# Optimization experiments

Measured on AMD Instinct MI355X. Metric: run time of the kernel, lower is better.

## Reference

```python
import jax, jax.numpy as jnp
import numpy as np

EPS = 1e-7  # K.epsilon()
ROUTINGS = 3


def squash(v, axis=-1):
    s2 = jnp.sum(jnp.square(v), axis=axis, keepdims=True)
    scale = s2 / (1.0 + s2) / jnp.sqrt(s2 + EPS)
    return scale * v


def setup_inputs() -> dict:
    key = jax.random.key(0)
    k1, k2 = jax.random.split(key)
    B, I, D_IN = 64, 2048, 16
    J, D_OUT = 32, 32
    inputs = jax.random.normal(k1, (B, I, D_IN), dtype=jnp.float32)
    W = jax.random.normal(k2, (J, I, D_OUT, D_IN), dtype=jnp.float32) * 0.05
    return {"inputs": inputs, "W": W}


def reference(inputs, W):
    # u_hat[b,j,i,e] = sum_d inputs[b,i,d] * W[j,i,e,d]
    u_hat = jnp.einsum('bid,jied->bjie', inputs, W)  # [B, J, I, D_out]
    B, J, I, _ = u_hat.shape
    b = jnp.zeros((B, J, I), dtype=u_hat.dtype)
    outputs = None
    for r in range(ROUTINGS):
        c = jax.nn.softmax(b, axis=1)                 # softmax over output capsules J
        s = jnp.einsum('bji,bjie->bje', c, u_hat)     # weighted sum over input capsules
        outputs = squash(s)                           # [B, J, D_out]
        if r < ROUTINGS - 1:
            b = b + jnp.einsum('bje,bjie->bji', outputs, u_hat)
    return outputs
```

## Files before the change

kernel.cpp:

```cpp
#include <hip/hip_runtime.h>
#include <hip/hip_bf16.h>

#define NB 64
#define NI 2048
#define ND 16
#define NJ 32
#define NE 32
#define NIP (NI/2)
#define NKC 64
#define NSL NKC

typedef __attribute__((ext_vector_type(8))) short bfrag;
typedef __attribute__((ext_vector_type(4))) float f32x4;

__device__ inline unsigned pk2bf(float a, float b) {
    __hip_bfloat162 h = __float22bfloat162_rn(make_float2(a, b));
    return *reinterpret_cast<unsigned*>(&h);
}

template <int N>
__device__ inline float rot16_add(float v) {
    int r = __builtin_amdgcn_mov_dpp(__float_as_int(v), 0x120 + N, 0xf, 0xf, false);
    return v + __int_as_float(r);
}

__device__ inline unsigned scale_pair(unsigned u, float cc) {
    float f0 = __uint_as_float(u << 16);
    float f1 = __uint_as_float(u & 0xffff0000u);
    return pk2bf(f0 * cc, f1 * cc);
}

__global__ __launch_bounds__(256) void convxT_k(const float* __restrict__ x,
                                                short* __restrict__ xT)
{
    const int T = blockIdx.x * 256 + threadIdx.x;
    const int i = T >> 6, b = T & 63;
    const float4* src = reinterpret_cast<const float4*>(
        x + ((size_t)b * NI + i) * ND);
    float4 a0 = src[0], a1 = src[1], a2 = src[2], a3 = src[3];
    bfrag lo, hi;
    unsigned* lu = reinterpret_cast<unsigned*>(&lo);
    unsigned* hu = reinterpret_cast<unsigned*>(&hi);
    lu[0] = pk2bf(a0.x, a0.y); lu[1] = pk2bf(a0.z, a0.w);
    lu[2] = pk2bf(a1.x, a1.y); lu[3] = pk2bf(a1.z, a1.w);
    hu[0] = pk2bf(a2.x, a2.y); hu[1] = pk2bf(a2.z, a2.w);
    hu[2] = pk2bf(a3.x, a3.y); hu[3] = pk2bf(a3.z, a3.w);
    short* dst = xT + ((size_t)i * NB + b) * ND;
    *reinterpret_cast<bfrag*>(dst)     = lo;
    *reinterpret_cast<bfrag*>(dst + 8) = hi;
}

__global__ __launch_bounds__(512) void lgsm_k(
    const short* __restrict__ xT,
    const short* __restrict__ Wb,
    const float* __restrict__ Oacc,
    float* __restrict__ c)
{
    const int l    = blockIdx.x;
    const int grp  = l >> 5;
    const int bb   = (l >> 3) & 3;
    const int ic   = grp * 8 + (l & 7);
    const int b0   = bb * 16;
    const int i0   = ic * 16;
    const int t    = threadIdx.x;
    const int wv   = t >> 6;
    const int ln   = t & 63;
    const int m    = ln & 15;
    const int quad = ln >> 4;

    __shared__ float lp[NJ][16][16];

    float O0[4][4], O1[4][4];
#pragma unroll
    for (int jj = 0; jj < 4; ++jj) {
        const int j = wv * 4 + jj;
#pragma unroll
        for (int r = 0; r < 4; ++r) {
            const int b = b0 + quad * 4 + r;
            O0[jj][r] = Oacc[((size_t)b * NJ + j) * NE + m];
            O1[jj][r] = Oacc[((size_t)b * NJ + j) * NE + 16 + m];
        }
    }

    const int  bA  = b0 + m;
    const bool act = quad < 2;
    const int  d0  = quad * 8;

    for (int il = 0; il < 16; ++il) {
        const int i = i0 + il;
        const int ip = i >> 1, isel = i & 1;
        bfrag av = (bfrag)0;
        if (act) {
            av = *reinterpret_cast<const bfrag*>(
                xT + ((size_t)i * NB + bA) * ND + d0);
        }
#pragma unroll
        for (int jj = 0; jj < 4; ++jj) {
            const int j = wv * 4 + jj;
            bfrag bv0 = (bfrag)0, bv1 = (bfrag)0;
            if (act) {
                const short* wp = Wb + (((size_t)j * NIP + ip) * NE + m) * 32
                                     + isel * 16 + d0;
                bv0 = *reinterpret_cast<const bfrag*>(wp);
                bv1 = *reinterpret_cast<const bfrag*>(wp + 16 * 32);
            }
            f32x4 z = {0.f, 0.f, 0.f, 0.f};
            f32x4 U0 = __builtin_amdgcn_mfma_f32_16x16x32_bf16(av, bv0, z, 0, 0, 0);
            f32x4 U1 = __builtin_amdgcn_mfma_f32_16x16x32_bf16(av, bv1, z, 0, 0, 0);

            float v4[4];
#pragma unroll
            for (int r = 0; r < 4; ++r) {
                float v = fmaf(U0[r], O0[jj][r], U1[r] * O1[jj][r]);
                v = rot16_add<1>(v);
                v = rot16_add<2>(v);
                v = rot16_add<4>(v);
                v = rot16_add<8>(v);
                v4[r] = v;
            }
            if (m == 0) {
                *reinterpret_cast<float4*>(&lp[j][il][quad * 4]) =
                    make_float4(v4[0], v4[1], v4[2], v4[3]);
            }
        }
    }
    __syncthreads();

    if (t < 256) {
        const int i = t >> 4, b = t & 15;
        float v[NJ];
        float mx = -1e30f;
#pragma unroll
        for (int jx = 0; jx < NJ; ++jx) {
            v[jx] = lp[jx][i][b];
            mx = fmaxf(mx, v[jx]);
        }
        float sum = 0.f;
#pragma unroll
        for (int jx = 0; jx < NJ; ++jx) {
            v[jx] = __expf(v[jx] - mx);
            sum += v[jx];
        }
        const float inv = 1.0f / sum;
#pragma unroll
        for (int jx = 0; jx < NJ; ++jx)
            c[((size_t)jx * NI + i0 + i) * NB + b0 + b] = v[jx] * inv;
    }
}


#define WS_LOAD(P, itv)                                                        \
    {   const int ip_ = ip0 + (itv);                                           \
        const int ia_ = ip_ * 2 + isel;                                        \
        if constexpr (R0) {                                                    \
            const float* wp_ = Wsrc + (((size_t)j * NI + ia_) * NE + m) * ND + d0; \
            P##w0 = *reinterpret_cast<const float4*>(wp_);                     \
            P##w1 = *reinterpret_cast<const float4*>(wp_ + 4);                 \
            P##w2 = *reinterpret_cast<const float4*>(wp_ + 16 * ND);           \
            P##w3 = *reinterpret_cast<const float4*>(wp_ + 16 * ND + 4);       \
        } else {                                                               \
            const short* bp_ = Wb + (((size_t)j * NIP + ip_) * NE + m) * 32 + quad * 8; \
            P##bv0 = *reinterpret_cast<const bfrag*>(bp_);                     \
            P##bv1 = *reinterpret_cast<const bfrag*>(bp_ + 512);               \
            const float* cp_ = cbuf + ((size_t)j * NI + ia_) * NB + m;         \
            P##c0 = cp_[0];  P##c1 = cp_[16];                                  \
            P##c2 = cp_[32]; P##c3 = cp_[48];                                  \
        }                                                                      \
        const short* xp_ = xT + ((size_t)ia_ * NB + m) * ND + d0;              \
        P##x0 = *reinterpret_cast<const uint4*>(xp_);                          \
        P##x1 = *reinterpret_cast<const uint4*>(xp_ + 16 * ND);                \
        P##x2 = *reinterpret_cast<const uint4*>(xp_ + 32 * ND);                \
        P##x3 = *reinterpret_cast<const uint4*>(xp_ + 48 * ND);                \
    }

#define WS_MT(XV, CV, A0, A1)                                                  \
    {   const float cc_ = R0 ? (1.0f / NJ) : (CV);                             \
        bfrag av_;                                                             \
        unsigned* au_ = reinterpret_cast<unsigned*>(&av_);                     \
        au_[0] = scale_pair((XV).x, cc_); au_[1] = scale_pair((XV).y, cc_);    \
        au_[2] = scale_pair((XV).z, cc_); au_[3] = scale_pair((XV).w, cc_);    \
        A0 = __builtin_amdgcn_mfma_f32_16x16x32_bf16(av_, bv0_, A0, 0, 0, 0);  \
        A1 = __builtin_amdgcn_mfma_f32_16x16x32_bf16(av_, bv1_, A1, 0, 0, 0);  \
    }

#define WS_COMPUTE(P, itv)                                                     \
    {   bfrag bv0_, bv1_;                                                      \
        if constexpr (R0) {                                                    \
            unsigned* b0_ = reinterpret_cast<unsigned*>(&bv0_);                \
            unsigned* b1_ = reinterpret_cast<unsigned*>(&bv1_);                \
            b0_[0] = pk2bf(P##w0.x, P##w0.y); b0_[1] = pk2bf(P##w0.z, P##w0.w);\
            b0_[2] = pk2bf(P##w1.x, P##w1.y); b0_[3] = pk2bf(P##w1.z, P##w1.w);\
            b1_[0] = pk2bf(P##w2.x, P##w2.y); b1_[1] = pk2bf(P##w2.z, P##w2.w);\
            b1_[2] = pk2bf(P##w3.x, P##w3.y); b1_[3] = pk2bf(P##w3.z, P##w3.w);\
            short* wd_ = Wb + (((size_t)j * NIP + (ip0 + (itv))) * NE + m) * 32 + quad * 8; \
            *reinterpret_cast<bfrag*>(wd_)       = bv0_;                       \
            *reinterpret_cast<bfrag*>(wd_ + 512) = bv1_;                       \
        } else { bv0_ = P##bv0; bv1_ = P##bv1; }                               \
        WS_MT(P##x0, P##c0, a00, a01)                                          \
        WS_MT(P##x1, P##c1, a10, a11)                                          \
        WS_MT(P##x2, P##c2, a20, a21)                                          \
        WS_MT(P##x3, P##c3, a30, a31)                                          \
    }

template <bool R0>
__global__ __launch_bounds__(128, 4) void wsum_k(
    const float* __restrict__ Wsrc,
    const short* __restrict__ xT,
    short* __restrict__ Wb,
    const float* __restrict__ cbuf,
    float* __restrict__ partial)
{
    const int l    = blockIdx.x;
    const int x    = l & 7;
    const int r    = l >> 3;
    const int j    = r & 31;
    const int kc   = x * 8 + (r >> 5);
    const int t    = threadIdx.x;
    const int wv   = t >> 6;
    const int ln   = t & 63;
    const int m    = ln & 15;
    const int quad = ln >> 4;
    const int isel = quad >> 1;
    const int d0   = (quad & 1) * 8;
    const int ip0  = kc * 16 + wv * 8;

    __shared__ float red[2][2048];

    f32x4 a00 = {0.f,0.f,0.f,0.f}, a01 = {0.f,0.f,0.f,0.f};
    f32x4 a10 = {0.f,0.f,0.f,0.f}, a11 = {0.f,0.f,0.f,0.f};
    f32x4 a20 = {0.f,0.f,0.f,0.f}, a21 = {0.f,0.f,0.f,0.f};
    f32x4 a30 = {0.f,0.f,0.f,0.f}, a31 = {0.f,0.f,0.f,0.f};

    bfrag  Abv0, Abv1, Bbv0, Bbv1;
    float4 Aw0, Aw1, Aw2, Aw3, Bw0, Bw1, Bw2, Bw3;
    uint4  Ax0, Ax1, Ax2, Ax3, Bx0, Bx1, Bx2, Bx3;
    float  Ac0, Ac1, Ac2, Ac3, Bc0, Bc1, Bc2, Bc3;

    WS_LOAD(A, 0)
    WS_LOAD(B, 1)
    WS_COMPUTE(A, 0)
    WS_LOAD(A, 2)
    WS_COMPUTE(B, 1)
    WS_LOAD(B, 3)
    WS_COMPUTE(A, 2)
    WS_LOAD(A, 4)
    WS_COMPUTE(B, 3)
    WS_LOAD(B, 5)
    WS_COMPUTE(A, 4)
    WS_LOAD(A, 6)
    WS_COMPUTE(B, 5)
    WS_LOAD(B, 7)
    WS_COMPUTE(A, 6)
    WS_COMPUTE(B, 7)

    float* rb = &red[wv][0];
    *reinterpret_cast<f32x4*>(rb + 0 * 256 + ln * 4) = a00;
    *reinterpret_cast<f32x4*>(rb + 1 * 256 + ln * 4) = a01;
    *reinterpret_cast<f32x4*>(rb + 2 * 256 + ln * 4) = a10;
    *reinterpret_cast<f32x4*>(rb + 3 * 256 + ln * 4) = a11;
    *reinterpret_cast<f32x4*>(rb + 4 * 256 + ln * 4) = a20;
    *reinterpret_cast<f32x4*>(rb + 5 * 256 + ln * 4) = a21;
    *reinterpret_cast<f32x4*>(rb + 6 * 256 + ln * 4) = a30;
    *reinterpret_cast<f32x4*>(rb + 7 * 256 + ln * 4) = a31;
    __syncthreads();

    float* pb = partial + ((size_t)kc * NJ + j) * 2048;
#pragma unroll
    for (int k = 0; k < 4; ++k) {
        const int g = k * 512 + t * 4;
        f32x4 s = *reinterpret_cast<const f32x4*>(&red[0][g]);
        s += *reinterpret_cast<const f32x4*>(&red[1][g]);
        *reinterpret_cast<f32x4*>(pb + g) = s;
    }
}

__global__ __launch_bounds__(512) void rs_k(
    const float* __restrict__ partial,
    float* __restrict__ Oacc,
    float* __restrict__ out,
    int mode)
{
    const int G    = blockIdx.x * 512 + threadIdx.x;
    const int j    = G >> 11;
    const int g    = G & 2047;
    const int group = g >> 8;
    const int mt   = group >> 1;
    const int nt   = group & 1;
    const int lnn  = (g >> 2) & 63;
    const int m    = lnn & 15;
    const int quad = lnn >> 4;
    const int r    = g & 3;
    const int b    = mt * 16 + quad * 4 + r;
    const int e    = nt * 16 + m;

    float sum = 0.f;
#pragma unroll 8
    for (int sl = 0; sl < NSL; ++sl)
        sum += partial[((size_t)sl * NJ + j) * 2048 + g];

    __shared__ float lds[512];
    const int row = quad * 4 + r;
    lds[row * 32 + e] = sum;
    __syncthreads();
    const float* rp = &lds[row * 32];
    float p = 0.f;
#pragma unroll
    for (int ee = 0; ee < 32; ++ee) p = fmaf(rp[ee], rp[ee], p);

    const float scale = p / ((1.0f + p) * sqrtf(p + 1e-7f));
    const float o = scale * sum;
    const size_t off = ((size_t)b * NJ + j) * NE + e;
    if (mode == 2)      out[off]  = o;
    else if (mode == 1) Oacc[off] += o;
    else                Oacc[off] = o;
}

extern "C" void kernel_launch(void* const* d_in, const int* in_sizes, int n_in,
                              void* d_out, int out_size, void* d_ws, size_t ws_size,
                              hipStream_t stream)
{
    (void)in_sizes; (void)n_in; (void)out_size; (void)ws_size;
    const float* x = (const float*)d_in[0];
    const float* W = (const float*)d_in[1];
    float* out = (float*)d_out;

    float* Oacc = (float*)d_ws;
    float* c    = Oacc + NB * NJ * NE;
    float* part = c + (size_t)NJ * NI * NB;
    short* Wb   = (short*)(part + (size_t)NSL * NJ * 2048);
    short* xT   = Wb + (size_t)NJ * NIP * NE * 32;

    convxT_k<<<(NI * NB) / 256, 256, 0, stream>>>(x, xT);

    wsum_k<true><<<NJ * NKC, 128, 0, stream>>>(W, xT, Wb, c, part);
    rs_k<<<65536 / 512, 512, 0, stream>>>(part, Oacc, out, 0);

    lgsm_k<<<512, 512, 0, stream>>>(xT, Wb, Oacc, c);
    wsum_k<false><<<NJ * NKC, 128, 0, stream>>>(W, xT, Wb, c, part);
    rs_k<<<65536 / 512, 512, 0, stream>>>(part, Oacc, out, 1);

    lgsm_k<<<512, 512, 0, stream>>>(xT, Wb, Oacc, c);
    wsum_k<false><<<NJ * NKC, 128, 0, stream>>>(W, xT, Wb, c, part);
    rs_k<<<65536 / 512, 512, 0, stream>>>(part, Oacc, out, 2);
}
```

Measured before the change: 339.1 us.

## Halve wsum K-chunk size to double block count and simplify reduction

Doubles the number of K-chunks, from 64 to 128, so each wsum block covers half as many input-capsule pairs (4 pipeline stages instead of 8). The grid gets twice the blocks for better CU occupancy and latency hiding. The cross-wave reduction now has wave 1 write its accumulators to a halved LDS buffer and wave 0 add them and write the partials. In exchange, partial traffic and the work in the downstream reduction over chunks double, and the occupancy hint is dropped from the launch bounds.

```diff
diff --git a/kernel.cpp b/kernel.cpp
--- a/kernel.cpp
+++ b/kernel.cpp
@@ -7,7 +7,7 @@
 #define NJ 32
 #define NE 32
 #define NIP (NI/2)
-#define NKC 64
+#define NKC 128
 #define NSL NKC
 
 typedef __attribute__((ext_vector_type(8))) short bfrag;
@@ -203,7 +203,7 @@
     }
 
 template <bool R0>
-__global__ __launch_bounds__(128, 4) void wsum_k(
+__global__ __launch_bounds__(128) void wsum_k(
     const float* __restrict__ Wsrc,
     const short* __restrict__ xT,
     short* __restrict__ Wb,
@@ -214,7 +214,7 @@
     const int x    = l & 7;
     const int r    = l >> 3;
     const int j    = r & 31;
-    const int kc   = x * 8 + (r >> 5);
+    const int kc   = x * 16 + (r >> 5);
     const int t    = threadIdx.x;
     const int wv   = t >> 6;
     const int ln   = t & 63;
@@ -222,9 +222,9 @@
     const int quad = ln >> 4;
     const int isel = quad >> 1;
     const int d0   = (quad & 1) * 8;
-    const int ip0  = kc * 16 + wv * 8;
-
-    __shared__ float red[2][2048];
+    const int ip0  = kc * 8 + wv * 4;
+
+    __shared__ float red[2048];
 
     f32x4 a00 = {0.f,0.f,0.f,0.f}, a01 = {0.f,0.f,0.f,0.f};
     f32x4 a10 = {0.f,0.f,0.f,0.f}, a11 = {0.f,0.f,0.f,0.f};
@@ -243,34 +243,38 @@
     WS_COMPUTE(B, 1)
     WS_LOAD(B, 3)
     WS_COMPUTE(A, 2)
-    WS_LOAD(A, 4)
     WS_COMPUTE(B, 3)
-    WS_LOAD(B, 5)
-    WS_COMPUTE(A, 4)
-    WS_LOAD(A, 6)
-    WS_COMPUTE(B, 5)
-    WS_LOAD(B, 7)
-    WS_COMPUTE(A, 6)
-    WS_COMPUTE(B, 7)
-
-    float* rb = &red[wv][0];
-    *reinterpret_cast<f32x4*>(rb + 0 * 256 + ln * 4) = a00;
-    *reinterpret_cast<f32x4*>(rb + 1 * 256 + ln * 4) = a01;
-    *reinterpret_cast<f32x4*>(rb + 2 * 256 + ln * 4) = a10;
-    *reinterpret_cast<f32x4*>(rb + 3 * 256 + ln * 4) = a11;
-    *reinterpret_cast<f32x4*>(rb + 4 * 256 + ln * 4) = a20;
-    *reinterpret_cast<f32x4*>(rb + 5 * 256 + ln * 4) = a21;
-    *reinterpret_cast<f32x4*>(rb + 6 * 256 + ln * 4) = a30;
-    *reinterpret_cast<f32x4*>(rb + 7 * 256 + ln * 4) = a31;
+
+    if (wv == 1) {
+        *reinterpret_cast<f32x4*>(red + 0 * 256 + ln * 4) = a00;
+        *reinterpret_cast<f32x4*>(red + 1 * 256 + ln * 4) = a01;
+        *reinterpret_cast<f32x4*>(red + 2 * 256 + ln * 4) = a10;
+        *reinterpret_cast<f32x4*>(red + 3 * 256 + ln * 4) = a11;
+        *reinterpret_cast<f32x4*>(red + 4 * 256 + ln * 4) = a20;
+        *reinterpret_cast<f32x4*>(red + 5 * 256 + ln * 4) = a21;
+        *reinterpret_cast<f32x4*>(red + 6 * 256 + ln * 4) = a30;
+        *reinterpret_cast<f32x4*>(red + 7 * 256 + ln * 4) = a31;
+    }
     __syncthreads();
 
-    float* pb = partial + ((size_t)kc * NJ + j) * 2048;
-#pragma unroll
-    for (int k = 0; k < 4; ++k) {
-        const int g = k * 512 + t * 4;
-        f32x4 s = *reinterpret_cast<const f32x4*>(&red[0][g]);
-        s += *reinterpret_cast<const f32x4*>(&red[1][g]);
-        *reinterpret_cast<f32x4*>(pb + g) = s;
+    if (wv == 0) {
+        float* pb = partial + ((size_t)kc * NJ + j) * 2048;
+        a00 += *reinterpret_cast<const f32x4*>(red + 0 * 256 + ln * 4);
+        a01 += *reinterpret_cast<const f32x4*>(red + 1 * 256 + ln * 4);
+        a10 += *reinterpret_cast<const f32x4*>(red + 2 * 256 + ln * 4);
+        a11 += *reinterpret_cast<const f32x4*>(red + 3 * 256 + ln * 4);
+        a20 += *reinterpret_cast<const f32x4*>(red + 4 * 256 + ln * 4);
+        a21 += *reinterpret_cast<const f32x4*>(red + 5 * 256 + ln * 4);
+        a30 += *reinterpret_cast<const f32x4*>(red + 6 * 256 + ln * 4);
+        a31 += *reinterpret_cast<const f32x4*>(red + 7 * 256 + ln * 4);
+        *reinterpret_cast<f32x4*>(pb + 0 * 256 + ln * 4) = a00;
+        *reinterpret_cast<f32x4*>(pb + 1 * 256 + ln * 4) = a01;
+        *reinterpret_cast<f32x4*>(pb + 2 * 256 + ln * 4) = a10;
+        *reinterpret_cast<f32x4*>(pb + 3 * 256 + ln * 4) = a11;
+        *reinterpret_cast<f32x4*>(pb + 4 * 256 + ln * 4) = a20;
+        *reinterpret_cast<f32x4*>(pb + 5 * 256 + ln * 4) = a21;
+        *reinterpret_cast<f32x4*>(pb + 6 * 256 + ln * 4) = a30;
+        *reinterpret_cast<f32x4*>(pb + 7 * 256 + ln * 4) = a31;
     }
 }
 
```

New measurement: 356.0 us. 1.05x slower.

## Fuse routing softmax with weighted-sum MFMA into one kernel per iteration

Applied to the files above, without the earlier changes.

Routing iterations 2 and 3 now use a single fused kernel. It computes the agreement logits, applies the softmax over output capsules in shared memory, and then reuses the same x and bf16 W tiles to accumulate the c-weighted sum with MFMA. Each iteration no longer writes and rereads the full coupling-coefficient buffer or makes a second pass over the bf16 W copy. A new reduction kernel sums the 32 per-block partials per output and applies squash. The trade-off is a larger partial buffer and a longer reduction, plus a second MFMA pass inside the fused kernel that adds register and shared-memory pressure.

```diff
diff --git a/kernel.cpp b/kernel.cpp
--- a/kernel.cpp
+++ b/kernel.cpp
@@ -50,11 +50,11 @@
     *reinterpret_cast<bfrag*>(dst + 8) = hi;
 }
 
-__global__ __launch_bounds__(512) void lgsm_k(
+__global__ __launch_bounds__(512) void fwd_k(
     const short* __restrict__ xT,
     const short* __restrict__ Wb,
     const float* __restrict__ Oacc,
-    float* __restrict__ c)
+    float* __restrict__ part)
 {
     const int l    = blockIdx.x;
     const int grp  = l >> 5;
@@ -68,7 +68,7 @@
     const int m    = ln & 15;
     const int quad = ln >> 4;
 
-    __shared__ float lp[NJ][16][16];
+    __shared__ float lsm[16][NJ][16];
 
     float O0[4][4], O1[4][4];
 #pragma unroll
@@ -119,7 +119,7 @@
                 v4[r] = v;
             }
             if (m == 0) {
-                *reinterpret_cast<float4*>(&lp[j][il][quad * 4]) =
+                *reinterpret_cast<float4*>(&lsm[il][j][quad * 4]) =
                     make_float4(v4[0], v4[1], v4[2], v4[3]);
             }
         }
@@ -127,24 +127,109 @@
     __syncthreads();
 
     if (t < 256) {
-        const int i = t >> 4, b = t & 15;
-        float v[NJ];
+        const int il = t >> 4, b = t & 15;
         float mx = -1e30f;
 #pragma unroll
+        for (int jx = 0; jx < NJ; ++jx) mx = fmaxf(mx, lsm[il][jx][b]);
+        float sum = 0.f;
+#pragma unroll
         for (int jx = 0; jx < NJ; ++jx) {
-            v[jx] = lp[jx][i][b];
-            mx = fmaxf(mx, v[jx]);
-        }
-        float sum = 0.f;
-#pragma unroll
-        for (int jx = 0; jx < NJ; ++jx) {
-            v[jx] = __expf(v[jx] - mx);
-            sum += v[jx];
+            const float e = __expf(lsm[il][jx][b] - mx);
+            lsm[il][jx][b] = e;
+            sum += e;
         }
         const float inv = 1.0f / sum;
 #pragma unroll
-        for (int jx = 0; jx < NJ; ++jx)
-            c[((size_t)jx * NI + i0 + i) * NB + b0 + b] = v[jx] * inv;
+        for (int jx = 0; jx < NJ; ++jx) lsm[il][jx][b] *= inv;
+    }
+    __syncthreads();
+
+    f32x4 acc0[4] = {{0.f,0.f,0.f,0.f},{0.f,0.f,0.f,0.f},
+                     {0.f,0.f,0.f,0.f},{0.f,0.f,0.f,0.f}};
+    f32x4 acc1[4] = {{0.f,0.f,0.f,0.f},{0.f,0.f,0.f,0.f},
+                     {0.f,0.f,0.f,0.f},{0.f,0.f,0.f,0.f}};
+    for (int il = 0; il < 16; ++il) {
+        const int i = i0 + il;
+        const int ip = i >> 1, isel = i & 1;
+        uint4 xr = {0u, 0u, 0u, 0u};
+        if (act) {
+            xr = *reinterpret_cast<const uint4*>(
+                xT + ((size_t)i * NB + bA) * ND + d0);
+        }
+#pragma unroll
+        for (int jj = 0; jj < 4; ++jj) {
+            const int j = wv * 4 + jj;
+            const float cv = lsm[il][j][m];
+            bfrag av2;
+            unsigned* au = reinterpret_cast<unsigned*>(&av2);
+            au[0] = scale_pair(xr.x, cv);
+            au[1] = scale_pair(xr.y, cv);
+            au[2] = scale_pair(xr.z, cv);
+            au[3] = scale_pair(xr.w, cv);
+            bfrag bv0 = (bfrag)0, bv1 = (bfrag)0;
+            if (act) {
+                const short* wp = Wb + (((size_t)j * NIP + ip) * NE + m) * 32
+                                     + isel * 16 + d0;
+                bv0 = *reinterpret_cast<const bfrag*>(wp);
+                bv1 = *reinterpret_cast<const bfrag*>(wp + 16 * 32);
+            }
+            acc0[jj] = __builtin_amdgcn_mfma_f32_16x16x32_bf16(av2, bv0, acc0[jj], 0, 0, 0);
+            acc1[jj] = __builtin_amdgcn_mfma_f32_16x16x32_bf16(av2, bv1, acc1[jj], 0, 0, 0);
+        }
+    }
+
+    float* base = part + ((size_t)(bb * 128 + ic) * NJ) * 512;
+#pragma unroll
+    for (int jj = 0; jj < 4; ++jj) {
+        const int j = wv * 4 + jj;
+#pragma unroll
+        for (int r = 0; r < 4; ++r) {
+            float* p = base + (size_t)j * 512 + (quad * 4 + r) * 32 + m;
+            p[0]  = acc0[jj][r];
+            p[16] = acc1[jj][r];
+        }
+    }
+}
+
+__global__ __launch_bounds__(512) void rs2_k(
+    const float* __restrict__ part,
+    float* __restrict__ Oacc,
+    float* __restrict__ out,
+    int mode)
+{
+    const int G2 = blockIdx.x * 512 + threadIdx.x;
+    const int row = G2 >> 2;
+    const int q   = G2 & 3;
+    const int e = row & 31, j = (row >> 5) & 31, b = row >> 10;
+    const int bb = b >> 4, bl = b & 15;
+
+    const float* p = part + ((size_t)(bb * 128 + q * 32) * NJ + j) * 512
+                          + bl * 32 + e;
+    float sum = 0.f;
+#pragma unroll 8
+    for (int s = 0; s < 32; ++s)
+        sum += p[(size_t)s * NJ * 512];
+
+    __shared__ float lds[512];
+    lds[threadIdx.x] = sum;
+    __syncthreads();
+
+    if (threadIdx.x < 128) {
+        const int t4 = threadIdx.x * 4;
+        const float s = lds[t4] + lds[t4 + 1] + lds[t4 + 2] + lds[t4 + 3];
+        const int row2 = blockIdx.x * 128 + threadIdx.x;
+        const int e2 = row2 & 31, j2 = (row2 >> 5) & 31, b2 = row2 >> 10;
+        float qq = s * s;
+        qq += __shfl_xor(qq, 1);
+        qq += __shfl_xor(qq, 2);
+        qq += __shfl_xor(qq, 4);
+        qq += __shfl_xor(qq, 8);
+        qq += __shfl_xor(qq, 16);
+        const float scale = qq / ((1.0f + qq) * sqrtf(qq + 1e-7f));
+        const float o = scale * s;
+        const size_t off = ((size_t)b2 * NJ + j2) * NE + e2;
+        if (mode == 2) out[off] = o;
+        else           Oacc[off] += o;
     }
 }
 
@@ -152,19 +237,12 @@
 #define WS_LOAD(P, itv)                                                        \
     {   const int ip_ = ip0 + (itv);                                           \
         const int ia_ = ip_ * 2 + isel;                                        \
-        if constexpr (R0) {                                                    \
+        {                                                                      \
             const float* wp_ = Wsrc + (((size_t)j * NI + ia_) * NE + m) * ND + d0; \
             P##w0 = *reinterpret_cast<const float4*>(wp_);                     \
             P##w1 = *reinterpret_cast<const float4*>(wp_ + 4);                 \
             P##w2 = *reinterpret_cast<const float4*>(wp_ + 16 * ND);           \
             P##w3 = *reinterpret_cast<const float4*>(wp_ + 16 * ND + 4);       \
-        } else {                                                               \
-            const short* bp_ = Wb + (((size_t)j * NIP + ip_) * NE + m) * 32 + quad * 8; \
-            P##bv0 = *reinterpret_cast<const bfrag*>(bp_);                     \
-            P##bv1 = *reinterpret_cast<const bfrag*>(bp_ + 512);               \
-            const float* cp_ = cbuf + ((size_t)j * NI + ia_) * NB + m;         \
-            P##c0 = cp_[0];  P##c1 = cp_[16];                                  \
-            P##c2 = cp_[32]; P##c3 = cp_[48];                                  \
         }                                                                      \
         const short* xp_ = xT + ((size_t)ia_ * NB + m) * ND + d0;              \
         P##x0 = *reinterpret_cast<const uint4*>(xp_);                          \
@@ -173,8 +251,8 @@
         P##x3 = *reinterpret_cast<const uint4*>(xp_ + 48 * ND);                \
     }
 
-#define WS_MT(XV, CV, A0, A1)                                                  \
-    {   const float cc_ = R0 ? (1.0f / NJ) : (CV);                             \
+#define WS_MT(XV, A0, A1)                                                      \
+    {   const float cc_ = 1.0f / NJ;                                           \
         bfrag av_;                                                             \
         unsigned* au_ = reinterpret_cast<unsigned*>(&av_);                     \
         au_[0] = scale_pair((XV).x, cc_); au_[1] = scale_pair((XV).y, cc_);    \
@@ -185,7 +263,7 @@
 
 #define WS_COMPUTE(P, itv)                                                     \
     {   bfrag bv0_, bv1_;                                                      \
-        if constexpr (R0) {                                                    \
+        {                                                                      \
             unsigned* b0_ = reinterpret_cast<unsigned*>(&bv0_);                \
             unsigned* b1_ = reinterpret_cast<unsigned*>(&bv1_);                \
             b0_[0] = pk2bf(P##w0.x, P##w0.y); b0_[1] = pk2bf(P##w0.z, P##w0.w);\
@@ -195,19 +273,17 @@
             short* wd_ = Wb + (((size_t)j * NIP + (ip0 + (itv))) * NE + m) * 32 + quad * 8; \
             *reinterpret_cast<bfrag*>(wd_)       = bv0_;                       \
             *reinterpret_cast<bfrag*>(wd_ + 512) = bv1_;                       \
-        } else { bv0_ = P##bv0; bv1_ = P##bv1; }                               \
-        WS_MT(P##x0, P##c0, a00, a01)                                          \
-        WS_MT(P##x1, P##c1, a10, a11)                                          \
-        WS_MT(P##x2, P##c2, a20, a21)                                          \
-        WS_MT(P##x3, P##c3, a30, a31)                                          \
-    }
-
-template <bool R0>
-__global__ __launch_bounds__(128, 4) void wsum_k(
+        }                                                                      \
+        WS_MT(P##x0, a00, a01)                                                 \
+        WS_MT(P##x1, a10, a11)                                                 \
+        WS_MT(P##x2, a20, a21)                                                 \
+        WS_MT(P##x3, a30, a31)                                                 \
+    }
+
+__global__ __launch_bounds__(128) void wsum_k(
     const float* __restrict__ Wsrc,
     const short* __restrict__ xT,
     short* __restrict__ Wb,
-    const float* __restrict__ cbuf,
     float* __restrict__ partial)
 {
     const int l    = blockIdx.x;
@@ -231,10 +307,8 @@
     f32x4 a20 = {0.f,0.f,0.f,0.f}, a21 = {0.f,0.f,0.f,0.f};
     f32x4 a30 = {0.f,0.f,0.f,0.f}, a31 = {0.f,0.f,0.f,0.f};
 
-    bfrag  Abv0, Abv1, Bbv0, Bbv1;
     float4 Aw0, Aw1, Aw2, Aw3, Bw0, Bw1, Bw2, Bw3;
     uint4  Ax0, Ax1, Ax2, Ax3, Bx0, Bx1, Bx2, Bx3;
-    float  Ac0, Ac1, Ac2, Ac3, Bc0, Bc1, Bc2, Bc3;
 
     WS_LOAD(A, 0)
     WS_LOAD(B, 1)
@@ -325,21 +399,18 @@
     float* out = (float*)d_out;
 
     float* Oacc = (float*)d_ws;
-    float* c    = Oacc + NB * NJ * NE;
-    float* part = c + (size_t)NJ * NI * NB;
-    short* Wb   = (short*)(part + (size_t)NSL * NJ * 2048);
+    float* part = Oacc + NB * NJ * NE;
+    short* Wb   = (short*)(part + (size_t)512 * NJ * 512);
     short* xT   = Wb + (size_t)NJ * NIP * NE * 32;
 
     convxT_k<<<(NI * NB) / 256, 256, 0, stream>>>(x, xT);
 
-    wsum_k<true><<<NJ * NKC, 128, 0, stream>>>(W, xT, Wb, c, part);
+    wsum_k<<<NJ * NKC, 128, 0, stream>>>(W, xT, Wb, part);
     rs_k<<<65536 / 512, 512, 0, stream>>>(part, Oacc, out, 0);
 
-    lgsm_k<<<512, 512, 0, stream>>>(xT, Wb, Oacc, c);
-    wsum_k<false><<<NJ * NKC, 128, 0, stream>>>(W, xT, Wb, c, part);
-    rs_k<<<65536 / 512, 512, 0, stream>>>(part, Oacc, out, 1);
-
-    lgsm_k<<<512, 512, 0, stream>>>(xT, Wb, Oacc, c);
-    wsum_k<false><<<NJ * NKC, 128, 0, stream>>>(W, xT, Wb, c, part);
-    rs_k<<<65536 / 512, 512, 0, stream>>>(part, Oacc, out, 2);
-}
+    fwd_k<<<512, 512, 0, stream>>>(xT, Wb, Oacc, part);
+    rs2_k<<<262144 / 512, 512, 0, stream>>>(part, Oacc, out, 1);
+
+    fwd_k<<<512, 512, 0, stream>>>(xT, Wb, Oacc, part);
+    rs2_k<<<262144 / 512, 512, 0, stream>>>(part, Oacc, out, 2);
+}
```

Result: slower. 359.0 us (+5.9%).
